# Optimization experiments

Hardware: AMD Instinct MI355X
Metric: run time of the kernel (lower is better)

## Reference

```python
import jax, jax.numpy as jnp
import numpy as np

B, S, D, H = 4, 2048, 1024, 16
DH = D // H
NEG = -1e6  # d2l masked_softmax fill value


def setup_inputs() -> dict:
    key = jax.random.key(0)
    kq, kk, kv, kl, k1, k2, k3, k4 = jax.random.split(key, 8)
    scale = 1.0 / np.sqrt(D)
    return {
        "queries": jax.random.normal(kq, (B, S, D), jnp.float32),
        "keys": jax.random.normal(kk, (B, S, D), jnp.float32),
        "values": jax.random.normal(kv, (B, S, D), jnp.float32),
        "valid_lens": jax.random.randint(kl, (B,), 1, S + 1, jnp.int32),
        "W_q": jax.random.normal(k1, (D, D), jnp.float32) * scale,
        "W_k": jax.random.normal(k2, (D, D), jnp.float32) * scale,
        "W_v": jax.random.normal(k3, (D, D), jnp.float32) * scale,
        "W_o": jax.random.normal(k4, (D, D), jnp.float32) * scale,
    }


def reference(queries, keys, values, valid_lens, W_q, W_k, W_v, W_o):
    # Linear projections (bias=False); torch Linear stores W as (out, in): y = x @ W.T
    def split_heads(x):  # (B,S,D) -> (B,H,S,DH)
        return x.reshape(B, S, H, DH).transpose(0, 2, 1, 3)

    q = split_heads(queries @ W_q.T)
    k = split_heads(keys @ W_k.T)
    v = split_heads(values @ W_v.T)

    scores = jnp.einsum("bhqd,bhkd->bhqk", q, k) / jnp.sqrt(jnp.float32(DH))
    # masked_softmax: mask key positions >= valid_len (per batch; repeat over heads == broadcast)
    key_mask = jnp.arange(S)[None, :] < valid_lens[:, None]  # (B,S)
    scores = jnp.where(key_mask[:, None, None, :], scores, NEG)
    attn = jax.nn.softmax(scores, axis=-1)
    out = jnp.einsum("bhqk,bhkd->bhqd", attn, v)
    out = out.transpose(0, 2, 1, 3).reshape(B, S, D)  # concat heads
    return out @ W_o.T
```

## Files before the change

### kernel.cpp

```cpp
#include <hip/hip_runtime.h>
#include <math.h>

#define BB 4
#define SS 2048
#define DD 1024
#define HH 16
#define DHH 64
#define NBH 64
#define SCC 0.18033688011112042f

typedef __attribute__((ext_vector_type(8))) short bf16x8;
typedef __attribute__((ext_vector_type(8))) unsigned short ushort8;
typedef __attribute__((ext_vector_type(4))) float f32x4;
typedef __attribute__((ext_vector_type(16))) float f32x16;
typedef __attribute__((ext_vector_type(2))) unsigned u32x2;
typedef unsigned short u16;

__device__ inline u16 f2bf(float x) {
    union { float f; unsigned u; } v; v.f = x;
    unsigned r = v.u + 0x7fffu + ((v.u >> 16) & 1u);
    return (u16)(r >> 16);
}

__device__ inline void gload16(const u16* g, u16* l) {
    __builtin_amdgcn_global_load_lds(
        (const __attribute__((address_space(1))) unsigned int*)(const void*)g,
        (__attribute__((address_space(3))) unsigned int*)(void*)l, 16, 0, 0);
}

__device__ inline void plswap(unsigned& a, unsigned& b) {
    u32x2 r = __builtin_amdgcn_permlane32_swap(a, b, false, false);
    a = r[0]; b = r[1];
}
__device__ inline float xhalf_max(float x) {
    u32x2 r = __builtin_amdgcn_permlane32_swap(
        __float_as_uint(x), __float_as_uint(x), false, false);
    return fmaxf(__uint_as_float(r[0]), __uint_as_float(r[1]));
}
__device__ inline float xhalf_sum(float x) {
    u32x2 r = __builtin_amdgcn_permlane32_swap(
        __float_as_uint(x), __float_as_uint(x), false, false);
    return __uint_as_float(r[0]) + __uint_as_float(r[1]);
}

__global__ __launch_bounds__(256)
void cvt_all(const float* __restrict__ q, const float* __restrict__ k,
             const float* __restrict__ v,
             const float* __restrict__ wq, const float* __restrict__ wk,
             const float* __restrict__ wv, const float* __restrict__ wo,
             const int* __restrict__ vlens,
             u16* __restrict__ oq, u16* __restrict__ ok, u16* __restrict__ ov,
             u16* __restrict__ owq, u16* __restrict__ owk,
             u16* __restrict__ owv, u16* __restrict__ owo)
{
    const int id = blockIdx.x;
    const float* s; u16* d; size_t i0;
    if (id < 12288) {
        const int y = id >> 12, xx = id & 4095;
        i0 = (size_t)xx * 2048;
        if (y == 0) { s = q; d = oq; }
        else if (y == 1) { s = k; d = ok; }
        else { s = v; d = ov; }
        if (y != 0) {
            const int b  = (int)(i0 >> 21);
            const int s0 = (int)(i0 >> 10) & (SS - 1);
            const int c32 = ((vlens[b] + 31) >> 5) << 5;
            if (s0 >= c32) return;
        }
    } else {
        const int r = id - 12288;
        const int y = r >> 9, xx = r & 511;
        i0 = (size_t)xx * 2048;
        if (y == 0) { s = wq; d = owq; }
        else if (y == 1) { s = wk; d = owk; }
        else if (y == 2) { s = wv; d = owv; }
        else { s = wo; d = owo; }
    }
    const size_t i = i0 + (size_t)threadIdx.x * 8;
    const float4 a = *(const float4*)(s + i);
    const float4 c = *(const float4*)(s + i + 4);
    ushort8 r;
    r[0] = f2bf(a.x); r[1] = f2bf(a.y); r[2] = f2bf(a.z); r[3] = f2bf(a.w);
    r[4] = f2bf(c.x); r[5] = f2bf(c.y); r[6] = f2bf(c.z); r[7] = f2bf(c.w);
    *(ushort8*)(d + i) = r;
}

__global__ __launch_bounds__(256)
void transpose_v(const u16* __restrict__ Vp, const int* __restrict__ vlens,
                 u16* __restrict__ Vt)
{
    __shared__ __align__(16) u16 tile[64][72];
    const int t = threadIdx.x;
    const int s0 = blockIdx.x * 64;
    const int bh = blockIdx.y;
    const int b  = bh >> 4;
    const int c32 = ((vlens[b] + 31) >> 5) << 5;
    if (s0 >= c32) return;
    const u16* src = Vp + ((size_t)bh * SS + s0) * DHH;
    const int r = t >> 2, d0 = (t & 3) * 16;
    *(ushort8*)&tile[r][d0]     = *(const ushort8*)(src + r * DHH + d0);
    *(ushort8*)&tile[r][d0 + 8] = *(const ushort8*)(src + r * DHH + d0 + 8);
    __syncthreads();
    const int d = t >> 2, sl = (t & 3) * 16;
    ushort8 o0, o1;
    #pragma unroll
    for (int j = 0; j < 8; ++j) o0[j] = tile[sl + j][d];
    #pragma unroll
    for (int j = 0; j < 8; ++j) o1[j] = tile[sl + 8 + j][d];
    u16* dst = Vt + ((size_t)bh * DHH + d) * SS + s0 + sl;
    *(ushort8*)dst       = o0;
    *(ushort8*)(dst + 8) = o1;
}

template<int OUT_MODE>
__device__ __forceinline__
void gemm_core(const u16* __restrict__ A, const u16* __restrict__ B,
               void* __restrict__ Cv, int m0, int n0, u16* As, u16* Bs)
{
    const int t = threadIdx.x;
    const int w = t >> 6, l = t & 63;
    const int lm = l & 15, lg = l >> 4;
    const int wr = w >> 1, wc = w & 1;

    const int lrow = l >> 3;
    const int lcb  = (l & 7) ^ lrow;
    const u16* ga = A + (size_t)(m0 + w * 32 + lrow) * DD + lcb * 8;
    const u16* gb = B + (size_t)(n0 + w * 32 + lrow) * DD + lcb * 8;
    u16* lA = &As[w * 2048];
    u16* lB = &Bs[w * 2048];

    f32x4 acc[4][4];
    #pragma unroll
    for (int i = 0; i < 4; ++i)
        #pragma unroll
        for (int j = 0; j < 4; ++j)
            acc[i][j] = (f32x4){0.f, 0.f, 0.f, 0.f};

    for (int k0 = 0; k0 < DD; k0 += 64) {
        __syncthreads();
        gload16(ga + k0,           lA);
        gload16(ga + k0 +  8 * DD, lA + 512);
        gload16(ga + k0 + 16 * DD, lA + 1024);
        gload16(ga + k0 + 24 * DD, lA + 1536);
        gload16(gb + k0,           lB);
        gload16(gb + k0 +  8 * DD, lB + 512);
        gload16(gb + k0 + 16 * DD, lB + 1024);
        gload16(gb + k0 + 24 * DD, lB + 1536);
        __syncthreads();
        #pragma unroll
        for (int kk = 0; kk < 2; ++kk) {
            bf16x8 af[4], bfr[4];
            #pragma unroll
            for (int mi = 0; mi < 4; ++mi) {
                const int R = wr * 64 + mi * 16 + lm;
                af[mi] = *(const bf16x8*)&As[R * 64 + (((kk * 4 + lg) ^ (R & 7)) * 8)];
            }
            #pragma unroll
            for (int ni = 0; ni < 4; ++ni) {
                const int R = wc * 64 + ni * 16 + lm;
                bfr[ni] = *(const bf16x8*)&Bs[R * 64 + (((kk * 4 + lg) ^ (R & 7)) * 8)];
            }
            #pragma unroll
            for (int mi = 0; mi < 4; ++mi)
                #pragma unroll
                for (int ni = 0; ni < 4; ++ni)
                    acc[mi][ni] = __builtin_amdgcn_mfma_f32_16x16x32_bf16(
                        af[mi], bfr[ni], acc[mi][ni], 0, 0, 0);
        }
    }

    #pragma unroll
    for (int mi = 0; mi < 4; ++mi) {
        #pragma unroll
        for (int r = 0; r < 4; ++r) {
            const int m = m0 + wr * 64 + mi * 16 + lg * 4 + r;
            if (OUT_MODE == 0) {
                float* C = (float*)Cv;
                #pragma unroll
                for (int ni = 0; ni < 4; ++ni)
                    C[(size_t)m * DD + n0 + wc * 64 + ni * 16 + lm] = acc[mi][ni][r];
            } else {
                u16* C = (u16*)Cv;
                const int b = m >> 11, s = m & (SS - 1);
                #pragma unroll
                for (int ni = 0; ni < 4; ++ni) {
                    const int n = n0 + wc * 64 + ni * 16 + lm;
                    const int h = n >> 6, dh = n & 63;
                    C[(((size_t)b * HH + h) * SS + s) * DHH + dh] = f2bf(acc[mi][ni][r]);
                }
            }
        }
    }
}

__global__ __launch_bounds__(256)
void gemm_qkv(const u16* __restrict__ Xq, const u16* __restrict__ Xk,
              const u16* __restrict__ Xv,
              const u16* __restrict__ Wqb, const u16* __restrict__ Wkb,
              const u16* __restrict__ Wvb,
              u16* __restrict__ Qo, u16* __restrict__ Ko, u16* __restrict__ Vo,
              const int* __restrict__ vlens)
{
    __shared__ __align__(16) u16 As[128 * 64];
    __shared__ __align__(16) u16 Bs[128 * 64];
    const int z = blockIdx.z;
    const int m0 = blockIdx.y * 128, n0 = blockIdx.x * 128;
    const u16* A; const u16* B; u16* C;
    if (z == 0) { A = Xq; B = Wqb; C = Qo; }
    else if (z == 1) { A = Xk; B = Wkb; C = Ko; }
    else { A = Xv; B = Wvb; C = Vo; }
    if (z != 0) {
        const int b = m0 >> 11, s0 = m0 & (SS - 1);
        const int c32 = ((vlens[b] + 31) >> 5) << 5;
        if (s0 >= c32) return;
    }
    gemm_core<1>(A, B, (void*)C, m0, n0, As, Bs);
}

__global__ __launch_bounds__(256)
void gemm_out(const u16* __restrict__ A, const u16* __restrict__ B,
              float* __restrict__ C)
{
    __shared__ __align__(16) u16 As[128 * 64];
    __shared__ __align__(16) u16 Bs[128 * 64];
    gemm_core<0>(A, B, (void*)C, blockIdx.y * 128, blockIdx.x * 128, As, Bs);
}

#define LOADK4(coff) do {                                                      \
    const u16* kp_ = kb + (size_t)(coff) * DHH;                                \
    kf[0] = *(const bf16x8*)kp_;                                               \
    kf[1] = *(const bf16x8*)(kp_ + 16);                                        \
    kf[2] = *(const bf16x8*)(kp_ + 32);                                        \
    kf[3] = *(const bf16x8*)(kp_ + 48);                                        \
} while (0)

#define LOADV4(coff) do {                                                      \
    const u16* vp_ = vb + (coff);                                              \
    va[0] = *(const bf16x8*)vp_;                                               \
    va[1] = *(const bf16x8*)(vp_ + 16);                                        \
    va[2] = *(const bf16x8*)(vp_ + (size_t)32 * SS);                           \
    va[3] = *(const bf16x8*)(vp_ + (size_t)32 * SS + 16);                      \
} while (0)

__global__ __launch_bounds__(64, 2)
void flash_mfma13(const u16* __restrict__ Qp, const u16* __restrict__ Kp,
                  const u16* __restrict__ Vt, const int* __restrict__ vlens,
                  u16* __restrict__ AO)
{
    const int l = threadIdx.x;
    const int l31 = l & 31, hi = l >> 5;
    const int x = blockIdx.x;
    const int xcd = x & 7;
    const int idx = x >> 3;
    const int bh  = xcd + ((idx >> 5) << 3);
    const int qpair = idx & 31;
    const int b = bh >> 4, h = bh & 15;
    const int q0 = qpair * 64;
    const int vlen = vlens[b];
    const int ntb = (vlen + 31) >> 5;

    const u16* qbA = Qp + ((size_t)bh * SS + q0 + l31) * DHH + hi * 8;
    bf16x8 qvA[4], qvB[4];
    qvA[0] = *(const bf16x8*)qbA;
    qvA[1] = *(const bf16x8*)(qbA + 16);
    qvA[2] = *(const bf16x8*)(qbA + 32);
    qvA[3] = *(const bf16x8*)(qbA + 48);
    const u16* qbB = qbA + (size_t)32 * DHH;
    qvB[0] = *(const bf16x8*)qbB;
    qvB[1] = *(const bf16x8*)(qbB + 16);
    qvB[2] = *(const bf16x8*)(qbB + 32);
    qvB[3] = *(const bf16x8*)(qbB + 48);

    const u16* kb = Kp + ((size_t)bh * SS + l31) * DHH + hi * 8;
    const u16* vb = Vt + ((size_t)bh * DHH + l31) * SS + hi * 8;

    bf16x8 kf[4], va[4];
    LOADK4(0);
    LOADV4(0);

    f32x16 oA0, oA1, oB0, oB1;
    #pragma unroll
    for (int r = 0; r < 16; ++r) { oA0[r] = 0.f; oA1[r] = 0.f; oB0[r] = 0.f; oB1[r] = 0.f; }
    float mA = -3e38f, lA = 0.f, mB = -3e38f, lB = 0.f;

    for (int tt = 0; tt < ntb; ++tt) {
        const int c0 = tt * 32;
        f32x16 zA, zB;
        #pragma unroll
        for (int r = 0; r < 16; ++r) { zA[r] = 0.f; zB[r] = 0.f; }
        __builtin_amdgcn_s_setprio(1);
        zA = __builtin_amdgcn_mfma_f32_32x32x16_bf16(kf[0], qvA[0], zA, 0, 0, 0);
        zB = __builtin_amdgcn_mfma_f32_32x32x16_bf16(kf[0], qvB[0], zB, 0, 0, 0);
        zA = __builtin_amdgcn_mfma_f32_32x32x16_bf16(kf[1], qvA[1], zA, 0, 0, 0);
        zB = __builtin_amdgcn_mfma_f32_32x32x16_bf16(kf[1], qvB[1], zB, 0, 0, 0);
        zA = __builtin_amdgcn_mfma_f32_32x32x16_bf16(kf[2], qvA[2], zA, 0, 0, 0);
        zB = __builtin_amdgcn_mfma_f32_32x32x16_bf16(kf[2], qvB[2], zB, 0, 0, 0);
        zA = __builtin_amdgcn_mfma_f32_32x32x16_bf16(kf[3], qvA[3], zA, 0, 0, 0);
        zB = __builtin_amdgcn_mfma_f32_32x32x16_bf16(kf[3], qvB[3], zB, 0, 0, 0);
        __builtin_amdgcn_s_setprio(0);
        if (tt + 1 < ntb) LOADK4(c0 + 32);

        if (vlen - c0 < 32) {
            #pragma unroll
            for (int r = 0; r < 16; ++r) {
                const int kvl = (r & 3) + 8 * (r >> 2) + 4 * hi;
                if (c0 + kvl >= vlen) { zA[r] = -3e38f; zB[r] = -3e38f; }
            }
        }

        float mxA = fmaxf(zA[0], zA[1]);
        float mxB = fmaxf(zB[0], zB[1]);
        #pragma unroll
        for (int r = 2; r < 16; ++r) { mxA = fmaxf(mxA, zA[r]); mxB = fmaxf(mxB, zB[r]); }
        mxA = xhalf_max(mxA);
        mxB = xhalf_max(mxB);

        float corrA = 1.f, corrB = 1.f;
        if (!__all(mxA <= mA + 64.0f)) {
            const float mold = mA;
            mA = fmaxf(mA, mxA);
            corrA = exp2f((mold - mA) * SCC);
            #pragma unroll
            for (int r = 0; r < 16; ++r) { oA0[r] *= corrA; oA1[r] *= corrA; }
        }
        if (!__all(mxB <= mB + 64.0f)) {
            const float mold = mB;
            mB = fmaxf(mB, mxB);
            corrB = exp2f((mold - mB) * SCC);
            #pragma unroll
            for (int r = 0; r < 16; ++r) { oB0[r] *= corrB; oB1[r] *= corrB; }
        }

        const float mscA = mA * SCC, mscB = mB * SCC;
        float tsA = 0.f, tsB = 0.f;
        #pragma unroll
        for (int r = 0; r < 16; ++r) {
            const float pA = exp2f(__builtin_fmaf(zA[r], SCC, -mscA));
            const float pB = exp2f(__builtin_fmaf(zB[r], SCC, -mscB));
            zA[r] = pA; zB[r] = pB;
            tsA += pA; tsB += pB;
        }
        tsA = xhalf_sum(tsA);
        tsB = xhalf_sum(tsB);
        lA = lA * corrA + tsA;
        lB = lB * corrB + tsB;

        unsigned a0, a1, a2, a3, a4, a5, a6, a7;
        unsigned b0, b1, b2, b3, b4, b5, b6, b7;
        asm("v_cvt_pk_bf16_f32 %0, %1, %2" : "=v"(a0) : "v"(zA[0]),  "v"(zA[1]));
        asm("v_cvt_pk_bf16_f32 %0, %1, %2" : "=v"(a1) : "v"(zA[2]),  "v"(zA[3]));
        asm("v_cvt_pk_bf16_f32 %0, %1, %2" : "=v"(a2) : "v"(zA[4]),  "v"(zA[5]));
        asm("v_cvt_pk_bf16_f32 %0, %1, %2" : "=v"(a3) : "v"(zA[6]),  "v"(zA[7]));
        asm("v_cvt_pk_bf16_f32 %0, %1, %2" : "=v"(a4) : "v"(zA[8]),  "v"(zA[9]));
        asm("v_cvt_pk_bf16_f32 %0, %1, %2" : "=v"(a5) : "v"(zA[10]), "v"(zA[11]));
        asm("v_cvt_pk_bf16_f32 %0, %1, %2" : "=v"(a6) : "v"(zA[12]), "v"(zA[13]));
        asm("v_cvt_pk_bf16_f32 %0, %1, %2" : "=v"(a7) : "v"(zA[14]), "v"(zA[15]));
        asm("v_cvt_pk_bf16_f32 %0, %1, %2" : "=v"(b0) : "v"(zB[0]),  "v"(zB[1]));
        asm("v_cvt_pk_bf16_f32 %0, %1, %2" : "=v"(b1) : "v"(zB[2]),  "v"(zB[3]));
        asm("v_cvt_pk_bf16_f32 %0, %1, %2" : "=v"(b2) : "v"(zB[4]),  "v"(zB[5]));
        asm("v_cvt_pk_bf16_f32 %0, %1, %2" : "=v"(b3) : "v"(zB[6]),  "v"(zB[7]));
        asm("v_cvt_pk_bf16_f32 %0, %1, %2" : "=v"(b4) : "v"(zB[8]),  "v"(zB[9]));
        asm("v_cvt_pk_bf16_f32 %0, %1, %2" : "=v"(b5) : "v"(zB[10]), "v"(zB[11]));
        asm("v_cvt_pk_bf16_f32 %0, %1, %2" : "=v"(b6) : "v"(zB[12]), "v"(zB[13]));
        asm("v_cvt_pk_bf16_f32 %0, %1, %2" : "=v"(b7) : "v"(zB[14]), "v"(zB[15]));

        plswap(a0, a2); plswap(a1, a3); plswap(a4, a6); plswap(a5, a7);
        plswap(b0, b2); plswap(b1, b3); plswap(b4, b6); plswap(b5, b7);

        bf16x8 pA0, pA1, pB0, pB1;
        ((unsigned*)&pA0)[0] = a0; ((unsigned*)&pA0)[1] = a1;
        ((unsigned*)&pA0)[2] = a2; ((unsigned*)&pA0)[3] = a3;
        ((unsigned*)&pA1)[0] = a4; ((unsigned*)&pA1)[1] = a5;
        ((unsigned*)&pA1)[2] = a6; ((unsigned*)&pA1)[3] = a7;
        ((unsigned*)&pB0)[0] = b0; ((unsigned*)&pB0)[1] = b1;
        ((unsigned*)&pB0)[2] = b2; ((unsigned*)&pB0)[3] = b3;
        ((unsigned*)&pB1)[0] = b4; ((unsigned*)&pB1)[1] = b5;
        ((unsigned*)&pB1)[2] = b6; ((unsigned*)&pB1)[3] = b7;

        __builtin_amdgcn_s_setprio(1);
        oA0 = __builtin_amdgcn_mfma_f32_32x32x16_bf16(va[0], pA0, oA0, 0, 0, 0);
        oB0 = __builtin_amdgcn_mfma_f32_32x32x16_bf16(va[0], pB0, oB0, 0, 0, 0);
        oA1 = __builtin_amdgcn_mfma_f32_32x32x16_bf16(va[2], pA0, oA1, 0, 0, 0);
        oB1 = __builtin_amdgcn_mfma_f32_32x32x16_bf16(va[2], pB0, oB1, 0, 0, 0);
        oA0 = __builtin_amdgcn_mfma_f32_32x32x16_bf16(va[1], pA1, oA0, 0, 0, 0);
        oB0 = __builtin_amdgcn_mfma_f32_32x32x16_bf16(va[1], pB1, oB0, 0, 0, 0);
        oA1 = __builtin_amdgcn_mfma_f32_32x32x16_bf16(va[3], pA1, oA1, 0, 0, 0);
        oB1 = __builtin_amdgcn_mfma_f32_32x32x16_bf16(va[3], pB1, oB1, 0, 0, 0);
        __builtin_amdgcn_s_setprio(0);
        if (tt + 1 < ntb) LOADV4(c0 + 32);
    }

    const float invA = 1.f / lA;
    const float invB = 1.f / lB;
    u16* obA = AO + ((size_t)b * SS + q0 + l31) * DD + h * DHH + hi * 4;
    u16* obB = obA + (size_t)32 * DD;
    #pragma unroll
    for (int rq = 0; rq < 4; ++rq) {
        #pragma unroll
        for (int rp = 0; rp < 2; ++rp) {
            const int r = rq * 4 + rp * 2;
            unsigned w0, w1, w2, w3;
            asm("v_cvt_pk_bf16_f32 %0, %1, %2" : "=v"(w0)
                : "v"(oA0[r] * invA), "v"(oA0[r + 1] * invA));
            asm("v_cvt_pk_bf16_f32 %0, %1, %2" : "=v"(w1)
                : "v"(oA1[r] * invA), "v"(oA1[r + 1] * invA));
            asm("v_cvt_pk_bf16_f32 %0, %1, %2" : "=v"(w2)
                : "v"(oB0[r] * invB), "v"(oB0[r + 1] * invB));
            asm("v_cvt_pk_bf16_f32 %0, %1, %2" : "=v"(w3)
                : "v"(oB1[r] * invB), "v"(oB1[r + 1] * invB));
            *(unsigned*)(obA + rq * 8 + rp * 2)      = w0;
            *(unsigned*)(obA + 32 + rq * 8 + rp * 2) = w1;
            *(unsigned*)(obB + rq * 8 + rp * 2)      = w2;
            *(unsigned*)(obB + 32 + rq * 8 + rp * 2) = w3;
        }
    }
}

extern "C" void kernel_launch(void* const* d_in, const int* in_sizes, int n_in,
                              void* d_out, int out_size, void* d_ws, size_t ws_size,
                              hipStream_t stream) {
    const float* queries = (const float*)d_in[0];
    const float* keys    = (const float*)d_in[1];
    const float* values  = (const float*)d_in[2];
    const int*   vlens   = (const int*)d_in[3];
    const float* Wq      = (const float*)d_in[4];
    const float* Wk      = (const float*)d_in[5];
    const float* Wv      = (const float*)d_in[6];
    const float* Wo      = (const float*)d_in[7];

    u16* ws = (u16*)d_ws;
    const size_t NX = (size_t)BB * SS * DD;
    const size_t NW = (size_t)DD * DD;
    u16* Xq  = ws;
    u16* Xk  = Xq  + NX;
    u16* Xv  = Xk  + NX;
    u16* Wqb = Xv  + NX;
    u16* Wkb = Wqb + NW;
    u16* Wvb = Wkb + NW;
    u16* Wob = Wvb + NW;
    u16* Qp  = Wob + NW;
    u16* Kp  = Qp  + NX;
    u16* Vp  = Kp  + NX;
    u16* Vtb = Vp  + NX;
    u16* AO  = Xq;

    cvt_all<<<dim3(14336), 256, 0, stream>>>(queries, keys, values,
                                             Wq, Wk, Wv, Wo, vlens,
                                             Xq, Xk, Xv, Wqb, Wkb, Wvb, Wob);

    gemm_qkv<<<dim3(DD / 128, (BB * SS) / 128, 3), 256, 0, stream>>>(
        Xq, Xk, Xv, Wqb, Wkb, Wvb, Qp, Kp, Vp, vlens);

    transpose_v<<<dim3(SS / 64, NBH), 256, 0, stream>>>(Vp, vlens, Vtb);
    flash_mfma13<<<dim3(2048), 64, 0, stream>>>(Qp, Kp, Vtb, vlens, AO);

    gemm_out<<<dim3(DD / 128, (BB * SS) / 128), 256, 0, stream>>>(AO, Wob, (float*)d_out);
}
```

Baseline: 191.9 us.

## Pair two batches per flash wave to balance variable valid lengths

Each wave now processes 32 query rows for the same head in two different batches (b=2p and 2p+1), instead of 64 query rows of one batch-head. Because valid_lens vary per batch, pairing batches evens out per-wave work, so fewer waves sit idle while a long-valid-length wave finishes. The cost is separate K/V streams per pair, since the two halves no longer share K/V fragments. That doubles K/V register fetches per MFMA and adds branches on per-batch activity flags.

```diff
diff --git a/kernel.cpp b/kernel.cpp
--- a/kernel.cpp
+++ b/kernel.cpp
@@ -226,24 +226,24 @@
     gemm_core<0>(A, B, (void*)C, blockIdx.y * 128, blockIdx.x * 128, As, Bs);
 }
 
-#define LOADK4(coff) do {                                                      \
-    const u16* kp_ = kb + (size_t)(coff) * DHH;                                \
-    kf[0] = *(const bf16x8*)kp_;                                               \
-    kf[1] = *(const bf16x8*)(kp_ + 16);                                        \
-    kf[2] = *(const bf16x8*)(kp_ + 32);                                        \
-    kf[3] = *(const bf16x8*)(kp_ + 48);                                        \
+#define LOADKX(KF, kbase, coff) do {                                           \
+    const u16* kp_ = (kbase) + (size_t)(coff) * DHH;                           \
+    KF[0] = *(const bf16x8*)kp_;                                               \
+    KF[1] = *(const bf16x8*)(kp_ + 16);                                        \
+    KF[2] = *(const bf16x8*)(kp_ + 32);                                        \
+    KF[3] = *(const bf16x8*)(kp_ + 48);                                        \
 } while (0)
 
-#define LOADV4(coff) do {                                                      \
-    const u16* vp_ = vb + (coff);                                              \
-    va[0] = *(const bf16x8*)vp_;                                               \
-    va[1] = *(const bf16x8*)(vp_ + 16);                                        \
-    va[2] = *(const bf16x8*)(vp_ + (size_t)32 * SS);                           \
-    va[3] = *(const bf16x8*)(vp_ + (size_t)32 * SS + 16);                      \
+#define LOADVX(VA, vbase, coff) do {                                           \
+    const u16* vp_ = (vbase) + (coff);                                         \
+    VA[0] = *(const bf16x8*)vp_;                                               \
+    VA[1] = *(const bf16x8*)(vp_ + 16);                                        \
+    VA[2] = *(const bf16x8*)(vp_ + (size_t)32 * SS);                           \
+    VA[3] = *(const bf16x8*)(vp_ + (size_t)32 * SS + 16);                      \
 } while (0)
 
 __global__ __launch_bounds__(64, 2)
-void flash_mfma13(const u16* __restrict__ Qp, const u16* __restrict__ Kp,
+void flash_mfma16(const u16* __restrict__ Qp, const u16* __restrict__ Kp,
                   const u16* __restrict__ Vt, const int* __restrict__ vlens,
                   u16* __restrict__ AO)
 {
@@ -252,148 +252,188 @@
     const int x = blockIdx.x;
     const int xcd = x & 7;
     const int idx = x >> 3;
-    const int bh  = xcd + ((idx >> 5) << 3);
-    const int qpair = idx & 31;
-    const int b = bh >> 4, h = bh & 15;
-    const int q0 = qpair * 64;
-    const int vlen = vlens[b];
-    const int ntb = (vlen + 31) >> 5;
-
-    const u16* qbA = Qp + ((size_t)bh * SS + q0 + l31) * DHH + hi * 8;
+    const int hbit = idx & 1;
+    const int p    = (idx >> 1) & 1;
+    const int qt   = idx >> 2;
+    const int h  = xcd + 8 * hbit;
+    const int bA = 2 * p, bB = 2 * p + 1;
+    const int bhA = bA * 16 + h, bhB = bB * 16 + h;
+    const int q0 = qt * 32;
+    const int vlenA = vlens[bA], vlenB = vlens[bB];
+    const int ntbA = (vlenA + 31) >> 5, ntbB = (vlenB + 31) >> 5;
+    const int ntbM = (ntbA > ntbB) ? ntbA : ntbB;
+
+    const u16* qbA = Qp + ((size_t)bhA * SS + q0 + l31) * DHH + hi * 8;
+    const u16* qbB = Qp + ((size_t)bhB * SS + q0 + l31) * DHH + hi * 8;
     bf16x8 qvA[4], qvB[4];
     qvA[0] = *(const bf16x8*)qbA;
     qvA[1] = *(const bf16x8*)(qbA + 16);
     qvA[2] = *(const bf16x8*)(qbA + 32);
     qvA[3] = *(const bf16x8*)(qbA + 48);
-    const u16* qbB = qbA + (size_t)32 * DHH;
     qvB[0] = *(const bf16x8*)qbB;
     qvB[1] = *(const bf16x8*)(qbB + 16);
     qvB[2] = *(const bf16x8*)(qbB + 32);
     qvB[3] = *(const bf16x8*)(qbB + 48);
 
-    const u16* kb = Kp + ((size_t)bh * SS + l31) * DHH + hi * 8;
-    const u16* vb = Vt + ((size_t)bh * DHH + l31) * SS + hi * 8;
-
-    bf16x8 kf[4], va[4];
-    LOADK4(0);
-    LOADV4(0);
+    const u16* kbA = Kp + ((size_t)bhA * SS + l31) * DHH + hi * 8;
+    const u16* kbB = Kp + ((size_t)bhB * SS + l31) * DHH + hi * 8;
+    const u16* vbA = Vt + ((size_t)bhA * DHH + l31) * SS + hi * 8;
+    const u16* vbB = Vt + ((size_t)bhB * DHH + l31) * SS + hi * 8;
+
+    bf16x8 kfA[4], kfB[4], vaA[4], vaB[4];
+    LOADKX(kfA, kbA, 0);
+    LOADKX(kfB, kbB, 0);
+    LOADVX(vaA, vbA, 0);
+    LOADVX(vaB, vbB, 0);
 
     f32x16 oA0, oA1, oB0, oB1;
     #pragma unroll
     for (int r = 0; r < 16; ++r) { oA0[r] = 0.f; oA1[r] = 0.f; oB0[r] = 0.f; oB1[r] = 0.f; }
     float mA = -3e38f, lA = 0.f, mB = -3e38f, lB = 0.f;
 
-    for (int tt = 0; tt < ntb; ++tt) {
+    for (int tt = 0; tt < ntbM; ++tt) {
         const int c0 = tt * 32;
+        const bool actA = tt < ntbA;
+        const bool actB = tt < ntbB;
+
         f32x16 zA, zB;
         #pragma unroll
         for (int r = 0; r < 16; ++r) { zA[r] = 0.f; zB[r] = 0.f; }
         __builtin_amdgcn_s_setprio(1);
-        zA = __builtin_amdgcn_mfma_f32_32x32x16_bf16(kf[0], qvA[0], zA, 0, 0, 0);
-        zB = __builtin_amdgcn_mfma_f32_32x32x16_bf16(kf[0], qvB[0], zB, 0, 0, 0);
-        zA = __builtin_amdgcn_mfma_f32_32x32x16_bf16(kf[1], qvA[1], zA, 0, 0, 0);
-        zB = __builtin_amdgcn_mfma_f32_32x32x16_bf16(kf[1], qvB[1], zB, 0, 0, 0);
-        zA = __builtin_amdgcn_mfma_f32_32x32x16_bf16(kf[2], qvA[2], zA, 0, 0, 0);
-        zB = __builtin_amdgcn_mfma_f32_32x32x16_bf16(kf[2], qvB[2], zB, 0, 0, 0);
-        zA = __builtin_amdgcn_mfma_f32_32x32x16_bf16(kf[3], qvA[3], zA, 0, 0, 0);
-        zB = __builtin_amdgcn_mfma_f32_32x32x16_bf16(kf[3], qvB[3], zB, 0, 0, 0);
+        if (actA) {
+            zA = __builtin_amdgcn_mfma_f32_32x32x16_bf16(kfA[0], qvA[0], zA, 0, 0, 0);
+            zA = __builtin_amdgcn_mfma_f32_32x32x16_bf16(kfA[1], qvA[1], zA, 0, 0, 0);
+            zA = __builtin_amdgcn_mfma_f32_32x32x16_bf16(kfA[2], qvA[2], zA, 0, 0, 0);
+            zA = __builtin_amdgcn_mfma_f32_32x32x16_bf16(kfA[3], qvA[3], zA, 0, 0, 0);
+        }
+        if (actB) {
+            zB = __builtin_amdgcn_mfma_f32_32x32x16_bf16(kfB[0], qvB[0], zB, 0, 0, 0);
+            zB = __builtin_amdgcn_mfma_f32_32x32x16_bf16(kfB[1], qvB[1], zB, 0, 0, 0);
+            zB = __builtin_amdgcn_mfma_f32_32x32x16_bf16(kfB[2], qvB[2], zB, 0, 0, 0);
+            zB = __builtin_amdgcn_mfma_f32_32x32x16_bf16(kfB[3], qvB[3], zB, 0, 0, 0);
+        }
         __builtin_amdgcn_s_setprio(0);
-        if (tt + 1 < ntb) LOADK4(c0 + 32);
-
-        if (vlen - c0 < 32) {
+        if (tt + 1 < ntbA) LOADKX(kfA, kbA, c0 + 32);
+        if (tt + 1 < ntbB) LOADKX(kfB, kbB, c0 + 32);
+
+        if (actA && vlenA - c0 < 32) {
             #pragma unroll
             for (int r = 0; r < 16; ++r) {
                 const int kvl = (r & 3) + 8 * (r >> 2) + 4 * hi;
-                if (c0 + kvl >= vlen) { zA[r] = -3e38f; zB[r] = -3e38f; }
-            }
-        }
-
-        float mxA = fmaxf(zA[0], zA[1]);
-        float mxB = fmaxf(zB[0], zB[1]);
-        #pragma unroll
-        for (int r = 2; r < 16; ++r) { mxA = fmaxf(mxA, zA[r]); mxB = fmaxf(mxB, zB[r]); }
-        mxA = xhalf_max(mxA);
-        mxB = xhalf_max(mxB);
-
-        float corrA = 1.f, corrB = 1.f;
-        if (!__all(mxA <= mA + 64.0f)) {
-            const float mold = mA;
-            mA = fmaxf(mA, mxA);
-            corrA = exp2f((mold - mA) * SCC);
-            #pragma unroll
-            for (int r = 0; r < 16; ++r) { oA0[r] *= corrA; oA1[r] *= corrA; }
-        }
-        if (!__all(mxB <= mB + 64.0f)) {
-            const float mold = mB;
-            mB = fmaxf(mB, mxB);
-            corrB = exp2f((mold - mB) * SCC);
-            #pragma unroll
-            for (int r = 0; r < 16; ++r) { oB0[r] *= corrB; oB1[r] *= corrB; }
-        }
-
-        const float mscA = mA * SCC, mscB = mB * SCC;
-        float tsA = 0.f, tsB = 0.f;
-        #pragma unroll
-        for (int r = 0; r < 16; ++r) {
-            const float pA = exp2f(__builtin_fmaf(zA[r], SCC, -mscA));
-            const float pB = exp2f(__builtin_fmaf(zB[r], SCC, -mscB));
-            zA[r] = pA; zB[r] = pB;
-            tsA += pA; tsB += pB;
-        }
-        tsA = xhalf_sum(tsA);
-        tsB = xhalf_sum(tsB);
-        lA = lA * corrA + tsA;
-        lB = lB * corrB + tsB;
-
-        unsigned a0, a1, a2, a3, a4, a5, a6, a7;
-        unsigned b0, b1, b2, b3, b4, b5, b6, b7;
-        asm("v_cvt_pk_bf16_f32 %0, %1, %2" : "=v"(a0) : "v"(zA[0]),  "v"(zA[1]));
-        asm("v_cvt_pk_bf16_f32 %0, %1, %2" : "=v"(a1) : "v"(zA[2]),  "v"(zA[3]));
-        asm("v_cvt_pk_bf16_f32 %0, %1, %2" : "=v"(a2) : "v"(zA[4]),  "v"(zA[5]));
-        asm("v_cvt_pk_bf16_f32 %0, %1, %2" : "=v"(a3) : "v"(zA[6]),  "v"(zA[7]));
-        asm("v_cvt_pk_bf16_f32 %0, %1, %2" : "=v"(a4) : "v"(zA[8]),  "v"(zA[9]));
-        asm("v_cvt_pk_bf16_f32 %0, %1, %2" : "=v"(a5) : "v"(zA[10]), "v"(zA[11]));
-        asm("v_cvt_pk_bf16_f32 %0, %1, %2" : "=v"(a6) : "v"(zA[12]), "v"(zA[13]));
-        asm("v_cvt_pk_bf16_f32 %0, %1, %2" : "=v"(a7) : "v"(zA[14]), "v"(zA[15]));
-        asm("v_cvt_pk_bf16_f32 %0, %1, %2" : "=v"(b0) : "v"(zB[0]),  "v"(zB[1]));
-        asm("v_cvt_pk_bf16_f32 %0, %1, %2" : "=v"(b1) : "v"(zB[2]),  "v"(zB[3]));
-        asm("v_cvt_pk_bf16_f32 %0, %1, %2" : "=v"(b2) : "v"(zB[4]),  "v"(zB[5]));
-        asm("v_cvt_pk_bf16_f32 %0, %1, %2" : "=v"(b3) : "v"(zB[6]),  "v"(zB[7]));
-        asm("v_cvt_pk_bf16_f32 %0, %1, %2" : "=v"(b4) : "v"(zB[8]),  "v"(zB[9]));
-        asm("v_cvt_pk_bf16_f32 %0, %1, %2" : "=v"(b5) : "v"(zB[10]), "v"(zB[11]));
-        asm("v_cvt_pk_bf16_f32 %0, %1, %2" : "=v"(b6) : "v"(zB[12]), "v"(zB[13]));
-        asm("v_cvt_pk_bf16_f32 %0, %1, %2" : "=v"(b7) : "v"(zB[14]), "v"(zB[15]));
-
-        plswap(a0, a2); plswap(a1, a3); plswap(a4, a6); plswap(a5, a7);
-        plswap(b0, b2); plswap(b1, b3); plswap(b4, b6); plswap(b5, b7);
-
-        bf16x8 pA0, pA1, pB0, pB1;
-        ((unsigned*)&pA0)[0] = a0; ((unsigned*)&pA0)[1] = a1;
-        ((unsigned*)&pA0)[2] = a2; ((unsigned*)&pA0)[3] = a3;
-        ((unsigned*)&pA1)[0] = a4; ((unsigned*)&pA1)[1] = a5;
-        ((unsigned*)&pA1)[2] = a6; ((unsigned*)&pA1)[3] = a7;
-        ((unsigned*)&pB0)[0] = b0; ((unsigned*)&pB0)[1] = b1;
-        ((unsigned*)&pB0)[2] = b2; ((unsigned*)&pB0)[3] = b3;
-        ((unsigned*)&pB1)[0] = b4; ((unsigned*)&pB1)[1] = b5;
-        ((unsigned*)&pB1)[2] = b6; ((unsigned*)&pB1)[3] = b7;
-
-        __builtin_amdgcn_s_setprio(1);
-        oA0 = __builtin_amdgcn_mfma_f32_32x32x16_bf16(va[0], pA0, oA0, 0, 0, 0);
-        oB0 = __builtin_amdgcn_mfma_f32_32x32x16_bf16(va[0], pB0, oB0, 0, 0, 0);
-        oA1 = __builtin_amdgcn_mfma_f32_32x32x16_bf16(va[2], pA0, oA1, 0, 0, 0);
-        oB1 = __builtin_amdgcn_mfma_f32_32x32x16_bf16(va[2], pB0, oB1, 0, 0, 0);
-        oA0 = __builtin_amdgcn_mfma_f32_32x32x16_bf16(va[1], pA1, oA0, 0, 0, 0);
-        oB0 = __builtin_amdgcn_mfma_f32_32x32x16_bf16(va[1], pB1, oB0, 0, 0, 0);
-        oA1 = __builtin_amdgcn_mfma_f32_32x32x16_bf16(va[3], pA1, oA1, 0, 0, 0);
-        oB1 = __builtin_amdgcn_mfma_f32_32x32x16_bf16(va[3], pB1, oB1, 0, 0, 0);
-        __builtin_amdgcn_s_setprio(0);
-        if (tt + 1 < ntb) LOADV4(c0 + 32);
+                if (c0 + kvl >= vlenA) zA[r] = -3e38f;
+            }
+        }
+        if (actB && vlenB - c0 < 32) {
+            #pragma unroll
+            for (int r = 0; r < 16; ++r) {
+                const int kvl = (r & 3) + 8 * (r >> 2) + 4 * hi;
+                if (c0 + kvl >= vlenB) zB[r] = -3e38f;
+            }
+        }
+
+        if (actA) {
+            float mx = fmaxf(zA[0], zA[1]);
+            #pragma unroll
+            for (int r = 2; r < 16; ++r) mx = fmaxf(mx, zA[r]);
+            mx = xhalf_max(mx);
+            float corr = 1.f;
+            if (!__all(mx <= mA + 64.0f)) {
+                const float mold = mA;
+                mA = fmaxf(mA, mx);
+                corr = exp2f((mold - mA) * SCC);
+                #pragma unroll
+                for (int r = 0; r < 16; ++r) { oA0[r] *= corr; oA1[r] *= corr; }
+            }
+            const float msc = mA * SCC;
+            float ts = 0.f;
+            #pragma unroll
+            for (int r = 0; r < 16; ++r) {
+                const float pv = exp2f(__builtin_fmaf(zA[r], SCC, -msc));
+                zA[r] = pv;
+                ts += pv;
+            }
+            ts = xhalf_sum(ts);
+            lA = lA * corr + ts;
+
+            unsigned a0, a1, a2, a3, a4, a5, a6, a7;
+            asm("v_cvt_pk_bf16_f32 %0, %1, %2" : "=v"(a0) : "v"(zA[0]),  "v"(zA[1]));
+            asm("v_cvt_pk_bf16_f32 %0, %1, %2" : "=v"(a1) : "v"(zA[2]),  "v"(zA[3]));
+            asm("v_cvt_pk_bf16_f32 %0, %1, %2" : "=v"(a2) : "v"(zA[4]),  "v"(zA[5]));
+            asm("v_cvt_pk_bf16_f32 %0, %1, %2" : "=v"(a3) : "v"(zA[6]),  "v"(zA[7]));
+            asm("v_cvt_pk_bf16_f32 %0, %1, %2" : "=v"(a4) : "v"(zA[8]),  "v"(zA[9]));
+            asm("v_cvt_pk_bf16_f32 %0, %1, %2" : "=v"(a5) : "v"(zA[10]), "v"(zA[11]));
+            asm("v_cvt_pk_bf16_f32 %0, %1, %2" : "=v"(a6) : "v"(zA[12]), "v"(zA[13]));
+            asm("v_cvt_pk_bf16_f32 %0, %1, %2" : "=v"(a7) : "v"(zA[14]), "v"(zA[15]));
+            plswap(a0, a2); plswap(a1, a3); plswap(a4, a6); plswap(a5, a7);
+            bf16x8 pA0, pA1;
+            ((unsigned*)&pA0)[0] = a0; ((unsigned*)&pA0)[1] = a1;
+            ((unsigned*)&pA0)[2] = a2; ((unsigned*)&pA0)[3] = a3;
+            ((unsigned*)&pA1)[0] = a4; ((unsigned*)&pA1)[1] = a5;
+            ((unsigned*)&pA1)[2] = a6; ((unsigned*)&pA1)[3] = a7;
+
+            __builtin_amdgcn_s_setprio(1);
+            oA0 = __builtin_amdgcn_mfma_f32_32x32x16_bf16(vaA[0], pA0, oA0, 0, 0, 0);
+            oA1 = __builtin_amdgcn_mfma_f32_32x32x16_bf16(vaA[2], pA0, oA1, 0, 0, 0);
+            oA0 = __builtin_amdgcn_mfma_f32_32x32x16_bf16(vaA[1], pA1, oA0, 0, 0, 0);
+            oA1 = __builtin_amdgcn_mfma_f32_32x32x16_bf16(vaA[3], pA1, oA1, 0, 0, 0);
+            __builtin_amdgcn_s_setprio(0);
+            if (tt + 1 < ntbA) LOADVX(vaA, vbA, c0 + 32);
+        }
+
+        if (actB) {
+            float mx = fmaxf(zB[0], zB[1]);
+            #pragma unroll
+            for (int r = 2; r < 16; ++r) mx = fmaxf(mx, zB[r]);
+            mx = xhalf_max(mx);
+            float corr = 1.f;
+            if (!__all(mx <= mB + 64.0f)) {
+                const float mold = mB;
+                mB = fmaxf(mB, mx);
+                corr = exp2f((mold - mB) * SCC);
+                #pragma unroll
+                for (int r = 0; r < 16; ++r) { oB0[r] *= corr; oB1[r] *= corr; }
+            }
+            const float msc = mB * SCC;
+            float ts = 0.f;
+            #pragma unroll
+            for (int r = 0; r < 16; ++r) {
+                const float pv = exp2f(__builtin_fmaf(zB[r], SCC, -msc));
+                zB[r] = pv;
+                ts += pv;
+            }
+            ts = xhalf_sum(ts);
+            lB = lB * corr + ts;
+
+            unsigned b0, b1, b2, b3, b4, b5, b6, b7;
+            asm("v_cvt_pk_bf16_f32 %0, %1, %2" : "=v"(b0) : "v"(zB[0]),  "v"(zB[1]));
+            asm("v_cvt_pk_bf16_f32 %0, %1, %2" : "=v"(b1) : "v"(zB[2]),  "v"(zB[3]));
+            asm("v_cvt_pk_bf16_f32 %0, %1, %2" : "=v"(b2) : "v"(zB[4]),  "v"(zB[5]));
+            asm("v_cvt_pk_bf16_f32 %0, %1, %2" : "=v"(b3) : "v"(zB[6]),  "v"(zB[7]));
+            asm("v_cvt_pk_bf16_f32 %0, %1, %2" : "=v"(b4) : "v"(zB[8]),  "v"(zB[9]));
+            asm("v_cvt_pk_bf16_f32 %0, %1, %2" : "=v"(b5) : "v"(zB[10]), "v"(zB[11]));
+            asm("v_cvt_pk_bf16_f32 %0, %1, %2" : "=v"(b6) : "v"(zB[12]), "v"(zB[13]));
+            asm("v_cvt_pk_bf16_f32 %0, %1, %2" : "=v"(b7) : "v"(zB[14]), "v"(zB[15]));
+            plswap(b0, b2); plswap(b1, b3); plswap(b4, b6); plswap(b5, b7);
+            bf16x8 pB0, pB1;
+            ((unsigned*)&pB0)[0] = b0; ((unsigned*)&pB0)[1] = b1;
+            ((unsigned*)&pB0)[2] = b2; ((unsigned*)&pB0)[3] = b3;
+            ((unsigned*)&pB1)[0] = b4; ((unsigned*)&pB1)[1] = b5;
+            ((unsigned*)&pB1)[2] = b6; ((unsigned*)&pB1)[3] = b7;
+
+            __builtin_amdgcn_s_setprio(1);
+            oB0 = __builtin_amdgcn_mfma_f32_32x32x16_bf16(vaB[0], pB0, oB0, 0, 0, 0);
+            oB1 = __builtin_amdgcn_mfma_f32_32x32x16_bf16(vaB[2], pB0, oB1, 0, 0, 0);
+            oB0 = __builtin_amdgcn_mfma_f32_32x32x16_bf16(vaB[1], pB1, oB0, 0, 0, 0);
+            oB1 = __builtin_amdgcn_mfma_f32_32x32x16_bf16(vaB[3], pB1, oB1, 0, 0, 0);
+            __builtin_amdgcn_s_setprio(0);
+            if (tt + 1 < ntbB) LOADVX(vaB, vbB, c0 + 32);
+        }
     }
 
     const float invA = 1.f / lA;
     const float invB = 1.f / lB;
-    u16* obA = AO + ((size_t)b * SS + q0 + l31) * DD + h * DHH + hi * 4;
-    u16* obB = obA + (size_t)32 * DD;
+    u16* obA = AO + ((size_t)bA * SS + q0 + l31) * DD + h * DHH + hi * 4;
+    u16* obB = AO + ((size_t)bB * SS + q0 + l31) * DD + h * DHH + hi * 4;
     #pragma unroll
     for (int rq = 0; rq < 4; ++rq) {
         #pragma unroll
@@ -452,7 +492,7 @@
         Xq, Xk, Xv, Wqb, Wkb, Wvb, Qp, Kp, Vp, vlens);
 
     transpose_v<<<dim3(SS / 64, NBH), 256, 0, stream>>>(Vp, vlens, Vtb);
-    flash_mfma13<<<dim3(2048), 64, 0, stream>>>(Qp, Kp, Vtb, vlens, AO);
+    flash_mfma16<<<dim3(2048), 64, 0, stream>>>(Qp, Kp, Vtb, vlens, AO);
 
     gemm_out<<<dim3(DD / 128, (BB * SS) / 128), 256, 0, stream>>>(AO, Wob, (float*)d_out);
 }
```

Result: slower. 256.6 us (+33.7%).
